# Kernel optimization log

Measured on AMD Instinct MI355X. Metric: run time of the kernel, lower is better.

## Reference

```python
import jax, jax.numpy as jnp
import numpy as np

B, L, H = 1024, 196, 1024  # batch, locations (14*14), hidden_size
A = 512                    # att_hid_size


def setup_inputs() -> dict:
    key = jax.random.key(0)
    ks = jax.random.split(key, 12)
    s = lambda k, shape, fan_in: jax.random.normal(k, shape, jnp.float32) / np.sqrt(fan_in)
    return {
        "att_features": jax.random.normal(ks[0], (B, L, H), jnp.float32),
        "h": jax.random.normal(ks[1], (B, H), jnp.float32),
        "W_att": s(ks[2], (H, A), H), "b_att": jnp.zeros((A,), jnp.float32),
        "W_h": s(ks[3], (H, A), H), "b_h": jnp.zeros((A,), jnp.float32),
        "w_alpha": s(ks[4], (A,), A), "b_alpha": jnp.zeros((), jnp.float32),
        "W_ch": s(ks[5], (L, A), L), "b_ch": jnp.zeros((A,), jnp.float32),
        "w_beta": s(ks[6], (A,), A), "b_beta": jnp.zeros((), jnp.float32),
    }


def reference(att_features, h, W_att, b_att, W_h, b_h, w_alpha, b_alpha,
              W_ch, b_ch, w_beta, b_beta):
    # spatial branch: project features [B,L,H] -> [B,L,A]
    spatial = jnp.einsum('blh,ha->bla', att_features, W_att) + b_att
    # channel branch: project location axis of [B,H,L] -> [B,H,A]
    channel = jnp.einsum('blh,la->bha', att_features, W_ch) + b_ch
    # query projection [B,A], broadcast over L (or H)
    p_h = (h @ W_h + b_h)[:, None, :]

    # spatial additive attention -> weights over L
    logits_s = jnp.einsum('bla,a->bl', jnp.tanh(spatial + p_h), w_alpha) + b_alpha
    w_spatial = jax.nn.softmax(logits_s, axis=1)                      # [B,L]
    weighted_spatial = jnp.einsum('bl,blh->bh', w_spatial, att_features)

    # channel additive attention -> weights over H
    logits_c = jnp.einsum('bha,a->bh', jnp.tanh(channel + p_h), w_beta) + b_beta
    w_channel = jax.nn.softmax(logits_c, axis=1)                      # [B,H]
    weighted_channel = jnp.einsum('bh,blh->bl', w_channel, att_features)

    return weighted_spatial, weighted_channel, w_spatial
```

## Files before the change

kernel.cpp:

```cpp
#include <hip/hip_runtime.h>
#include <cstdint>
#include <cstddef>


#define DEVI __device__ __forceinline__

typedef __bf16 bf16;
typedef bf16 bf16x4 __attribute__((ext_vector_type(4)));
typedef bf16 bf16x8 __attribute__((ext_vector_type(8)));
typedef float f32x4 __attribute__((ext_vector_type(4)));
typedef unsigned int uint32;

static constexpr int Bb = 1024;
static constexpr int Ll = 196;
static constexpr int Hh = 1024;
static constexpr int BL = Bb * Ll;

#define LGKM0     asm volatile("s_waitcnt lgkmcnt(0)" ::: "memory")
#define SBAR()    __builtin_amdgcn_s_barrier()
#define SCHED0()  __builtin_amdgcn_sched_barrier(0)

DEVI float fast_tanh(float x) {
  float e = __expf(2.f * x);
  return 1.f - 2.f * __builtin_amdgcn_rcpf(e + 1.f);
}

DEVI uint32 packbf2(float a, float b) {
  union { bf16 h; unsigned short u; } x, y;
  x.h = (bf16)a; y.h = (bf16)b;
  return (uint32)x.u | ((uint32)y.u << 16);
}

__global__ void k_build_wt(const float* __restrict__ W, bf16* __restrict__ P) {
  int idx = blockIdx.x * 256 + threadIdx.x;
  int a = idx & 511;
  int ko = (idx >> 9) << 3;
  bf16x8 v;
#pragma unroll
  for (int j = 0; j < 8; ++j) v[j] = (bf16)W[(size_t)(ko + j) * 512 + a];
  int panel = ko >> 5;
  int slot = ((ko >> 3) & 3) ^ ((a >> 1) & 3);
  *reinterpret_cast<bf16x8*>((char*)P + (size_t)panel * 32768 + a * 64 + slot * 16) = v;
}

__global__ void k_build_wct(const float* __restrict__ W, bf16* __restrict__ P) {
  int idx = blockIdx.x * 256 + threadIdx.x;
  int a = idx & 511;
  int lo = (idx >> 9) << 3;
  bf16x8 v;
#pragma unroll
  for (int j = 0; j < 8; ++j)
    v[j] = (lo + j < Ll) ? (bf16)W[(size_t)(lo + j) * 512 + a] : (bf16)0.f;
  int panel = lo >> 5;
  int slot = ((lo >> 3) & 3) ^ ((a >> 1) & 3);
  *reinterpret_cast<bf16x8*>((char*)P + (size_t)panel * 32768 + a * 64 + slot * 16) = v;
}

__global__ void k_ph(const float* __restrict__ h, const float* __restrict__ W_h,
                     const float* __restrict__ b_h, float* __restrict__ p_h) {
  int a = blockIdx.x * 256 + threadIdx.x;
  int b0 = blockIdx.y * 8;
  float acc[8] = {0.f, 0.f, 0.f, 0.f, 0.f, 0.f, 0.f, 0.f};
  for (int k = 0; k < 1024; ++k) {
    float w = W_h[(size_t)k * 512 + a];
#pragma unroll
    for (int i = 0; i < 8; ++i) acc[i] += h[(size_t)(b0 + i) * 1024 + k] * w;
  }
#pragma unroll
  for (int i = 0; i < 8; ++i) p_h[(size_t)(b0 + i) * 512 + a] = acc[i] + b_h[a];
}

#define SPA(p) ((p) * 5120)
#define SP_ASTR 80
__launch_bounds__(512)
__global__ void k_spatial(const float* __restrict__ att, const bf16* __restrict__ WtP,
                          const float* __restrict__ b_att, const float* __restrict__ p_h,
                          const float* __restrict__ w_alpha, float* __restrict__ logits_s) {
  __shared__ alignas(1024) char lds[12288];
  const int tid = threadIdx.x;
  const int lane = tid & 63;
  const int wn = tid >> 6;
  const int l15 = lane & 15, l4 = lane >> 4;
  const size_t row0 = (size_t)blockIdx.x * 64;
  const int slotP = (l4 ^ ((l15 >> 1) & 3)) << 4;
  const int ar = tid >> 3;
  const int aks = (tid & 7) << 2;
  const char* WtPc = (const char*)WtP;
  const float* apbase = att + (row0 + ar) * 1024 + aks;
  int boff[4];
#pragma unroll
  for (int n = 0; n < 4; ++n) boff[n] = (wn * 64 + n * 16 + l15) * 64 + slotP;

  f32x4 acc[4][4];
#pragma unroll
  for (int m = 0; m < 4; ++m)
#pragma unroll
    for (int n = 0; n < 4; ++n) acc[m][n] = f32x4{0.f, 0.f, 0.f, 0.f};

  float4 c0x = *reinterpret_cast<const float4*>(apbase);
  float4 c1x = *reinterpret_cast<const float4*>(apbase + 32);
  {
    bf16x4 w0 = {(bf16)c0x.x, (bf16)c0x.y, (bf16)c0x.z, (bf16)c0x.w};
    *reinterpret_cast<bf16x4*>(&lds[SPA(0) + ar * SP_ASTR + (aks << 1)]) = w0;
  }
  c0x = *reinterpret_cast<const float4*>(apbase + 64);
  LGKM0;
  SCHED0();
  SBAR();
  SCHED0();

  for (int t = 0; t < 32; ++t) {
    const int p = t & 1;
    const char* bpan = WtPc + (size_t)t * 32768;
    bf16x8 bv[4];
#pragma unroll
    for (int n = 0; n < 4; ++n)
      bv[n] = *reinterpret_cast<const bf16x8*>(bpan + boff[n]);
    bf16x8 af[4];
#pragma unroll
    for (int m = 0; m < 4; ++m)
      af[m] = *reinterpret_cast<const bf16x8*>(
          &lds[SPA(p) + (m * 16 + l15) * SP_ASTR + (l4 << 4)]);
    if (t < 31) {
      const int awoff = SPA(p ^ 1) + ar * SP_ASTR + (aks << 1);
      if ((t & 1) == 0) {
        bf16x4 w0 = {(bf16)c1x.x, (bf16)c1x.y, (bf16)c1x.z, (bf16)c1x.w};
        *reinterpret_cast<bf16x4*>(&lds[awoff]) = w0;
        if (t <= 28)
          c1x = *reinterpret_cast<const float4*>(apbase + (t + 3) * 32);
      } else {
        bf16x4 w0 = {(bf16)c0x.x, (bf16)c0x.y, (bf16)c0x.z, (bf16)c0x.w};
        *reinterpret_cast<bf16x4*>(&lds[awoff]) = w0;
        if (t <= 28)
          c0x = *reinterpret_cast<const float4*>(apbase + (t + 3) * 32);
      }
    }
#pragma unroll
    for (int n = 0; n < 4; ++n)
#pragma unroll
      for (int m = 0; m < 4; ++m)
        acc[m][n] = __builtin_amdgcn_mfma_f32_16x16x32_bf16(af[m], bv[n], acc[m][n], 0, 0, 0);
    LGKM0;
    SCHED0();
    SBAR();
    SCHED0();
  }

  float wa[4], ba[4], ph0[4], ph1[4];
  unsigned b0i = (unsigned)row0 / 196u;
  unsigned b1i = (unsigned)(row0 + 63) / 196u;
  unsigned bnd = (b0i + 1) * 196u;
#pragma unroll
  for (int n = 0; n < 4; ++n) {
    int a = wn * 64 + n * 16 + l15;
    wa[n] = w_alpha[a];
    ba[n] = b_att[a];
    ph0[n] = p_h[(size_t)b0i * 512 + a];
    ph1[n] = p_h[(size_t)b1i * 512 + a];
  }
  float* red = reinterpret_cast<float*>(lds);
#pragma unroll
  for (int m = 0; m < 4; ++m) {
#pragma unroll
    for (int j = 0; j < 4; ++j) {
      int rloc = m * 16 + l4 * 4 + j;
      unsigned R = (unsigned)row0 + rloc;
      bool hib = R >= bnd;
      float s = 0.f;
#pragma unroll
      for (int n = 0; n < 4; ++n)
        s += fast_tanh(acc[m][n][j] + ba[n] + (hib ? ph1[n] : ph0[n])) * wa[n];
      s += __shfl_xor(s, 1);
      s += __shfl_xor(s, 2);
      s += __shfl_xor(s, 4);
      s += __shfl_xor(s, 8);
      if (l15 == 0) red[wn * 64 + rloc] = s;
    }
  }
  __syncthreads();
  if (tid < 64) {
    float r = 0.f;
#pragma unroll
    for (int w = 0; w < 8; ++w) r += red[w * 64 + tid];
    logits_s[row0 + tid] = r;
  }
}

#define CT_STR 464
#define CH_PHC 59392
#define CH_WB  61440
__launch_bounds__(512)
__global__ void k_channel(const float* __restrict__ att, const bf16* __restrict__ WctP,
                          const float* __restrict__ b_ch, const float* __restrict__ p_h,
                          const float* __restrict__ w_beta, float* __restrict__ logits_c) {
  __shared__ alignas(1024) char lds[63488];
  const int tid = threadIdx.x;
  const int lane = tid & 63;
  const int wn = tid >> 6;
  const int l15 = lane & 15, l4 = lane >> 4;
  const int b = blockIdx.y;
  const int h0 = blockIdx.x * 128;
  const float* attb = att + (size_t)b * Ll * 1024 + h0;
  const char* Pc = (const char*)WctP;
  const int slotP = (l4 ^ ((l15 >> 1) & 3)) << 4;
  const int slotT = (l4 ^ ((l15 >> 2) & 3)) << 4;
  int poff0 = (wn * 32 + l15) * 64 + slotP;
  int poff1 = (wn * 32 + 16 + l15) * 64 + slotP;

  float pr = p_h[(size_t)b * 512 + tid];
  float bc = b_ch[tid];
  float wb = w_beta[tid];
  bf16x8 avC0 = *reinterpret_cast<const bf16x8*>(Pc + poff0);
  bf16x8 avC1 = *reinterpret_cast<const bf16x8*>(Pc + poff1);
  {
    const int grp = tid >> 8;
    const int t2 = tid & 255;
    const int lp = t2 >> 4;
    const int hq = (t2 & 15) << 2;
    const int usw = lp ^ ((t2 & 3) << 2);
    const int ch0 = grp ? 4 : 0;
    const int nch = grp ? 3 : 4;
#pragma unroll
    for (int hh = 0; hh < 2; ++hh) {
      const int hb = hq + 64 * hh;
      float4 va[4], vb[4];
#pragma unroll
      for (int i = 0; i < 4; ++i) {
        if (i >= nch) break;
        int ch = ch0 + i;
        int lg = ch * 32 + 2 * lp;
        va[i] = float4{0.f, 0.f, 0.f, 0.f};
        vb[i] = float4{0.f, 0.f, 0.f, 0.f};
        if (lg < Ll)
          va[i] = *reinterpret_cast<const float4*>(&attb[(size_t)lg * 1024 + hb]);
        if (lg + 1 < Ll)
          vb[i] = *reinterpret_cast<const float4*>(&attb[(size_t)(lg + 1) * 1024 + hb]);
      }
#pragma unroll
      for (int i = 0; i < 4; ++i) {
        if (i >= nch) break;
        int ch = ch0 + i;
        uint32 pk[4] = {packbf2(va[i].x, vb[i].x), packbf2(va[i].y, vb[i].y),
                        packbf2(va[i].z, vb[i].z), packbf2(va[i].w, vb[i].w)};
#pragma unroll
        for (int c = 0; c < 4; ++c)
          *reinterpret_cast<uint32*>(
              &lds[(hb + c) * CT_STR + ch * 64 + 4 * usw]) = pk[c];
      }
    }
  }
  {
    float* phcL = reinterpret_cast<float*>(&lds[CH_PHC]);
    float* wbL = reinterpret_cast<float*>(&lds[CH_WB]);
    phcL[tid] = pr + bc;
    wbL[tid] = wb;
  }

  f32x4 acc[2][8];
#pragma unroll
  for (int m = 0; m < 2; ++m)
#pragma unroll
    for (int n = 0; n < 8; ++n) acc[m][n] = f32x4{0.f, 0.f, 0.f, 0.f};
  float sn[8] = {0.f, 0.f, 0.f, 0.f, 0.f, 0.f, 0.f, 0.f};
  const float* phcLc = reinterpret_cast<const float*>(&lds[CH_PHC]);
  const float* wbLc = reinterpret_cast<const float*>(&lds[CH_WB]);

  LGKM0;
  SCHED0();
  SBAR();
  SCHED0();

#pragma unroll 1
  for (int s = 0; s < 14; ++s) {
    const int tk = (s >= 7) ? s - 7 : s;
    bf16x8 avN0 = avC0, avN1 = avC1;
    if (s < 13) {
      const int s1 = s + 1;
      const char* pan = Pc + (size_t)((s1 >= 7) ? s1 - 7 : s1) * 32768 +
                        ((s1 >= 7) ? 16384 : 0);
      avN0 = *reinterpret_cast<const bf16x8*>(pan + poff0);
      avN1 = *reinterpret_cast<const bf16x8*>(pan + poff1);
    }
#pragma unroll
    for (int half = 0; half < 2; ++half) {
      bf16x8 bv[4];
#pragma unroll
      for (int q = 0; q < 4; ++q)
        bv[q] = *reinterpret_cast<const bf16x8*>(
            &lds[((half * 4 + q) * 16 + l15) * CT_STR + tk * 64 + slotT]);
#pragma unroll
      for (int q = 0; q < 4; ++q) {
        acc[0][half * 4 + q] =
            __builtin_amdgcn_mfma_f32_16x16x32_bf16(avC0, bv[q], acc[0][half * 4 + q], 0, 0, 0);
        acc[1][half * 4 + q] =
            __builtin_amdgcn_mfma_f32_16x16x32_bf16(avC1, bv[q], acc[1][half * 4 + q], 0, 0, 0);
      }
    }
    if (s == 6) {
#pragma unroll
      for (int m = 0; m < 2; ++m) {
        int abase = wn * 32 + m * 16 + l4 * 4;
        float4 p4 = *reinterpret_cast<const float4*>(&phcLc[abase]);
        float4 w4 = *reinterpret_cast<const float4*>(&wbLc[abase]);
#pragma unroll
        for (int n = 0; n < 8; ++n) {
          sn[n] += fast_tanh(acc[m][n][0] + p4.x) * w4.x;
          sn[n] += fast_tanh(acc[m][n][1] + p4.y) * w4.y;
          sn[n] += fast_tanh(acc[m][n][2] + p4.z) * w4.z;
          sn[n] += fast_tanh(acc[m][n][3] + p4.w) * w4.w;
          acc[m][n] = f32x4{0.f, 0.f, 0.f, 0.f};
        }
      }
    }
    avC0 = avN0;
    avC1 = avN1;
  }
#pragma unroll
  for (int m = 0; m < 2; ++m) {
    int abase = 256 + wn * 32 + m * 16 + l4 * 4;
    float4 p4 = *reinterpret_cast<const float4*>(&phcLc[abase]);
    float4 w4 = *reinterpret_cast<const float4*>(&wbLc[abase]);
#pragma unroll
    for (int n = 0; n < 8; ++n) {
      sn[n] += fast_tanh(acc[m][n][0] + p4.x) * w4.x;
      sn[n] += fast_tanh(acc[m][n][1] + p4.y) * w4.y;
      sn[n] += fast_tanh(acc[m][n][2] + p4.z) * w4.z;
      sn[n] += fast_tanh(acc[m][n][3] + p4.w) * w4.w;
    }
  }
#pragma unroll
  for (int n = 0; n < 8; ++n) {
    sn[n] += __shfl_xor(sn[n], 16);
    sn[n] += __shfl_xor(sn[n], 32);
  }
  __syncthreads();
  float* red = reinterpret_cast<float*>(lds);
  if (l4 == 0) {
#pragma unroll
    for (int n = 0; n < 8; ++n) red[wn * 128 + n * 16 + l15] = sn[n];
  }
  __syncthreads();
  if (tid < 128) {
    float r = 0.f;
#pragma unroll
    for (int w = 0; w < 8; ++w) r += red[w * 128 + tid];
    logits_c[(size_t)b * 1024 + h0 + tid] = r;
  }
}

__launch_bounds__(512)
__global__ void k_weighted(const float* __restrict__ att, const float* __restrict__ logits_s,
                           const float* __restrict__ logits_c, float* __restrict__ out_s,
                           float* __restrict__ out_c, float* __restrict__ out_wsp) {
  __shared__ float wsl[Ll];
  __shared__ float chan[8][Ll];
  __shared__ float wchan[1024];
  __shared__ float4 acmbA[256];
  __shared__ float4 acmbB[256];
  __shared__ float sm[16];
  const int t = threadIdx.x, lane = t & 63, wn = t >> 6;
  const int t2 = t & 255, g = t >> 8;
  const int b = blockIdx.x;

  float xs = (t < Ll) ? logits_s[(size_t)b * Ll + t] : -1e30f;
  float m = xs;
#pragma unroll
  for (int o = 32; o; o >>= 1) m = fmaxf(m, __shfl_xor(m, o));
  if (lane == 0) sm[wn] = m;
  __syncthreads();
  m = fmaxf(fmaxf(fmaxf(sm[0], sm[1]), fmaxf(sm[2], sm[3])),
            fmaxf(fmaxf(sm[4], sm[5]), fmaxf(sm[6], sm[7])));
  float es = (t < Ll) ? __expf(xs - m) : 0.f;
  float ss = es;
#pragma unroll
  for (int o = 32; o; o >>= 1) ss += __shfl_xor(ss, o);
  if (lane == 0) sm[8 + wn] = ss;
  __syncthreads();
  ss = (sm[8] + sm[9]) + (sm[10] + sm[11]) + (sm[12] + sm[13]) + (sm[14] + sm[15]);
  if (t < Ll) {
    float w = es / ss;
    wsl[t] = w;
    out_wsp[(size_t)b * Ll + t] = w;
  }
  __syncthreads();

  float2 xc = *reinterpret_cast<const float2*>(&logits_c[(size_t)b * 1024 + 2 * t]);
  float mc = fmaxf(xc.x, xc.y);
#pragma unroll
  for (int o = 32; o; o >>= 1) mc = fmaxf(mc, __shfl_xor(mc, o));
  if (lane == 0) sm[wn] = mc;
  __syncthreads();
  mc = fmaxf(fmaxf(fmaxf(sm[0], sm[1]), fmaxf(sm[2], sm[3])),
             fmaxf(fmaxf(sm[4], sm[5]), fmaxf(sm[6], sm[7])));
  float e0 = __expf(xc.x - mc), e1 = __expf(xc.y - mc);
  float cs = e0 + e1;
#pragma unroll
  for (int o = 32; o; o >>= 1) cs += __shfl_xor(cs, o);
  if (lane == 0) sm[8 + wn] = cs;
  __syncthreads();
  cs = (sm[8] + sm[9]) + (sm[10] + sm[11]) + (sm[12] + sm[13]) + (sm[14] + sm[15]);
  float rcs = 1.f / cs;
  wchan[2 * t] = e0 * rcs;
  wchan[2 * t + 1] = e1 * rcs;
  __syncthreads();

  float4 wc4 = *reinterpret_cast<const float4*>(&wchan[4 * t2]);
  const float* attb = att + (size_t)b * Ll * 1024;
  float4 accs = {0.f, 0.f, 0.f, 0.f};
  for (int l = g; l < Ll; l += 2) {
    float4 v = *reinterpret_cast<const float4*>(&attb[(size_t)l * 1024 + 4 * t2]);
    float w = wsl[l];
    accs.x += w * v.x; accs.y += w * v.y; accs.z += w * v.z; accs.w += w * v.w;
    float pc = wc4.x * v.x + wc4.y * v.y + wc4.z * v.z + wc4.w * v.w;
#pragma unroll
    for (int o = 32; o; o >>= 1) pc += __shfl_xor(pc, o);
    if (lane == 0) chan[wn][l] = pc;
  }
  (g == 0 ? acmbA : acmbB)[t2] = accs;
  __syncthreads();
  if (t < 256) {
    float4 a = acmbA[t], c = acmbB[t];
    float4 o4 = {a.x + c.x, a.y + c.y, a.z + c.z, a.w + c.w};
    *reinterpret_cast<float4*>(&out_s[(size_t)b * 1024 + 4 * t]) = o4;
  }
  if (t < Ll) {
    int gg = (t & 1) * 4;
    out_c[(size_t)b * Ll + t] =
        (chan[gg][t] + chan[gg + 1][t]) + (chan[gg + 2][t] + chan[gg + 3][t]);
  }
}

extern "C" void kernel_launch(void* const* d_in, const int* in_sizes, int n_in,
                              void* d_out, int out_size, void* d_ws, size_t ws_size,
                              hipStream_t stream) {
  (void)in_sizes; (void)n_in; (void)out_size; (void)ws_size;
  const float* att     = (const float*)d_in[0];
  const float* h       = (const float*)d_in[1];
  const float* W_att   = (const float*)d_in[2];
  const float* b_att   = (const float*)d_in[3];
  const float* W_h     = (const float*)d_in[4];
  const float* b_h     = (const float*)d_in[5];
  const float* w_alpha = (const float*)d_in[6];
  const float* W_ch    = (const float*)d_in[8];
  const float* b_ch    = (const float*)d_in[9];
  const float* w_beta  = (const float*)d_in[10];

  float* out_ws    = (float*)d_out;
  float* out_wc    = out_ws + (size_t)Bb * Hh;
  float* out_wspat = out_wc + (size_t)Bb * Ll;

  char* ws = (char*)d_ws;
  float* p_h      = (float*)(ws);
  float* logits_s = (float*)(ws + 2097152);
  float* logits_c = (float*)(ws + 2899968);
  bf16*  WtP      = (bf16*)(ws + 11288576);
  bf16*  WctP     = (bf16*)(ws + 12337152);

  k_build_wt<<<256, 256, 0, stream>>>(W_att, WtP);
  k_build_wct<<<56, 256, 0, stream>>>(W_ch, WctP);
  k_ph<<<dim3(2, 128), 256, 0, stream>>>(h, W_h, b_h, p_h);
  k_spatial<<<BL / 64, 512, 0, stream>>>(att, WtP, b_att, p_h, w_alpha, logits_s);
  k_channel<<<dim3(8, 1024), 512, 0, stream>>>(att, WctP, b_ch, p_h, w_beta, logits_c);
  k_weighted<<<1024, 512, 0, stream>>>(att, logits_s, logits_c, out_ws, out_wc, out_wspat);
}
```

Before: 919.8 us.

## Stage eight A k-tiles per barrier phase and prefetch next B panel in registers

The spatial projection kernel used to double-buffer one 32-wide k-tile of activations in LDS and sync at every tile. It now loads eight k-tiles of fp32 activations at once, converts them to bf16 and writes them into a larger LDS buffer. It then runs eight MFMA steps with a single barrier per phase, while prefetching the next weight panel from global memory into registers one step ahead. The goal is fewer barriers and less exposed global latency, paid for with more LDS (40KB), more registers and a bulk load stall at the start of each phase with no overlap.

```diff
diff --git a/kernel.cpp b/kernel.cpp
--- a/kernel.cpp
+++ b/kernel.cpp
@@ -70,13 +70,13 @@
   for (int i = 0; i < 8; ++i) p_h[(size_t)(b0 + i) * 512 + a] = acc[i] + b_h[a];
 }
 
-#define SPA(p) ((p) * 5120)
 #define SP_ASTR 80
+#define SP_ST   5120
 __launch_bounds__(512)
 __global__ void k_spatial(const float* __restrict__ att, const bf16* __restrict__ WtP,
                           const float* __restrict__ b_att, const float* __restrict__ p_h,
                           const float* __restrict__ w_alpha, float* __restrict__ logits_s) {
-  __shared__ alignas(1024) char lds[12288];
+  __shared__ alignas(1024) char lds[40960];
   const int tid = threadIdx.x;
   const int lane = tid & 63;
   const int wn = tid >> 6;
@@ -87,6 +87,7 @@
   const int aks = (tid & 7) << 2;
   const char* WtPc = (const char*)WtP;
   const float* apbase = att + (row0 + ar) * 1024 + aks;
+  const int awoff = ar * SP_ASTR + (aks << 1);
   int boff[4];
 #pragma unroll
   for (int n = 0; n < 4; ++n) boff[n] = (wn * 64 + n * 16 + l15) * 64 + slotP;
@@ -97,49 +98,53 @@
 #pragma unroll
     for (int n = 0; n < 4; ++n) acc[m][n] = f32x4{0.f, 0.f, 0.f, 0.f};
 
-  float4 c0x = *reinterpret_cast<const float4*>(apbase);
-  float4 c1x = *reinterpret_cast<const float4*>(apbase + 32);
-  {
-    bf16x4 w0 = {(bf16)c0x.x, (bf16)c0x.y, (bf16)c0x.z, (bf16)c0x.w};
-    *reinterpret_cast<bf16x4*>(&lds[SPA(0) + ar * SP_ASTR + (aks << 1)]) = w0;
-  }
-  c0x = *reinterpret_cast<const float4*>(apbase + 64);
-  LGKM0;
-  SCHED0();
-  SBAR();
-  SCHED0();
-
-  for (int t = 0; t < 32; ++t) {
-    const int p = t & 1;
-    const char* bpan = WtPc + (size_t)t * 32768;
-    bf16x8 bv[4];
-#pragma unroll
-    for (int n = 0; n < 4; ++n)
-      bv[n] = *reinterpret_cast<const bf16x8*>(bpan + boff[n]);
-    bf16x8 af[4];
-#pragma unroll
-    for (int m = 0; m < 4; ++m)
-      af[m] = *reinterpret_cast<const bf16x8*>(
-          &lds[SPA(p) + (m * 16 + l15) * SP_ASTR + (l4 << 4)]);
-    if (t < 31) {
-      const int awoff = SPA(p ^ 1) + ar * SP_ASTR + (aks << 1);
-      if ((t & 1) == 0) {
-        bf16x4 w0 = {(bf16)c1x.x, (bf16)c1x.y, (bf16)c1x.z, (bf16)c1x.w};
-        *reinterpret_cast<bf16x4*>(&lds[awoff]) = w0;
-        if (t <= 28)
-          c1x = *reinterpret_cast<const float4*>(apbase + (t + 3) * 32);
-      } else {
-        bf16x4 w0 = {(bf16)c0x.x, (bf16)c0x.y, (bf16)c0x.z, (bf16)c0x.w};
-        *reinterpret_cast<bf16x4*>(&lds[awoff]) = w0;
-        if (t <= 28)
-          c0x = *reinterpret_cast<const float4*>(apbase + (t + 3) * 32);
-      }
-    }
-#pragma unroll
-    for (int n = 0; n < 4; ++n)
+  bf16x8 bvC0 = *reinterpret_cast<const bf16x8*>(WtPc + boff[0]);
+  bf16x8 bvC1 = *reinterpret_cast<const bf16x8*>(WtPc + boff[1]);
+  bf16x8 bvC2 = *reinterpret_cast<const bf16x8*>(WtPc + boff[2]);
+  bf16x8 bvC3 = *reinterpret_cast<const bf16x8*>(WtPc + boff[3]);
+
+#pragma unroll 1
+  for (int ph = 0; ph < 4; ++ph) {
+    {
+      float4 c[8];
+#pragma unroll
+      for (int st = 0; st < 8; ++st)
+        c[st] = *reinterpret_cast<const float4*>(apbase + ph * 256 + st * 32);
+#pragma unroll
+      for (int st = 0; st < 8; ++st) {
+        bf16x4 w0 = {(bf16)c[st].x, (bf16)c[st].y, (bf16)c[st].z, (bf16)c[st].w};
+        *reinterpret_cast<bf16x4*>(&lds[st * SP_ST + awoff]) = w0;
+      }
+    }
+    LGKM0;
+    SCHED0();
+    SBAR();
+    SCHED0();
+#pragma unroll 1
+    for (int st = 0; st < 8; ++st) {
+      const int t = ph * 8 + st;
+      bf16x8 bvN0 = bvC0, bvN1 = bvC1, bvN2 = bvC2, bvN3 = bvC3;
+      if (t < 31) {
+        const char* bpan = WtPc + (size_t)(t + 1) * 32768;
+        bvN0 = *reinterpret_cast<const bf16x8*>(bpan + boff[0]);
+        bvN1 = *reinterpret_cast<const bf16x8*>(bpan + boff[1]);
+        bvN2 = *reinterpret_cast<const bf16x8*>(bpan + boff[2]);
+        bvN3 = *reinterpret_cast<const bf16x8*>(bpan + boff[3]);
+      }
+      bf16x8 af[4];
 #pragma unroll
       for (int m = 0; m < 4; ++m)
-        acc[m][n] = __builtin_amdgcn_mfma_f32_16x16x32_bf16(af[m], bv[n], acc[m][n], 0, 0, 0);
+        af[m] = *reinterpret_cast<const bf16x8*>(
+            &lds[st * SP_ST + (m * 16 + l15) * SP_ASTR + (l4 << 4)]);
+#pragma unroll
+      for (int m = 0; m < 4; ++m) {
+        acc[m][0] = __builtin_amdgcn_mfma_f32_16x16x32_bf16(af[m], bvC0, acc[m][0], 0, 0, 0);
+        acc[m][1] = __builtin_amdgcn_mfma_f32_16x16x32_bf16(af[m], bvC1, acc[m][1], 0, 0, 0);
+        acc[m][2] = __builtin_amdgcn_mfma_f32_16x16x32_bf16(af[m], bvC2, acc[m][2], 0, 0, 0);
+        acc[m][3] = __builtin_amdgcn_mfma_f32_16x16x32_bf16(af[m], bvC3, acc[m][3], 0, 0, 0);
+      }
+      bvC0 = bvN0; bvC1 = bvN1; bvC2 = bvN2; bvC3 = bvN3;
+    }
     LGKM0;
     SCHED0();
     SBAR();
```

Result: faster. 896.7 us (-2.5%).
